# Optimization experiments

Hardware: AMD Instinct MI355X
Metric: run time of the kernel (lower is better)

The kernel has to match this reference:

```python
import jax, jax.numpy as jnp
import numpy as np
import math

B, N, D, H = 32, 577, 768, 12
HD = D // H  # 64
WS = 24  # window size
NUM_REL_DIST = (2 * WS - 1) * (2 * WS - 1) + 3  # 2212


def _build_rel_pos_index():
    ch, cw = np.arange(WS), np.arange(WS)
    coords = np.stack(np.meshgrid(ch, cw, indexing='ij'))  # [2, WS, WS]
    cf = coords.reshape(2, -1)  # [2, WS*WS]
    rel = cf[:, :, None] - cf[:, None, :]  # [2, WS*WS, WS*WS]
    rel = rel.transpose(1, 2, 0).astype(np.int64)
    rel[:, :, 0] += WS - 1
    rel[:, :, 1] += WS - 1
    rel[:, :, 0] *= 2 * WS - 1
    idx = np.zeros((WS * WS + 1, WS * WS + 1), dtype=np.int64)
    idx[1:, 1:] = rel.sum(-1)
    idx[0, 0:] = NUM_REL_DIST - 3
    idx[0:, 0] = NUM_REL_DIST - 2
    idx[0, 0] = NUM_REL_DIST - 1
    return idx.astype(np.int32)


def setup_inputs() -> dict:
    key = jax.random.key(0)
    ks = jax.random.split(key, 7)
    s = 1.0 / math.sqrt(D)
    return {
        'hidden_states': jax.random.normal(ks[0], (B, N, D), jnp.float32),
        'q_w': jax.random.normal(ks[1], (D, D), jnp.float32) * s,
        'q_b': jax.random.normal(ks[2], (D,), jnp.float32) * 0.02,
        'k_w': jax.random.normal(ks[3], (D, D), jnp.float32) * s,
        'v_w': jax.random.normal(ks[4], (D, D), jnp.float32) * s,
        'v_b': jax.random.normal(ks[5], (D,), jnp.float32) * 0.02,
        'rel_pos_table': jax.random.normal(ks[6], (NUM_REL_DIST, H), jnp.float32) * 0.02,
        'rel_pos_index': jnp.asarray(_build_rel_pos_index()),
    }


def reference(hidden_states, q_w, q_b, k_w, v_w, v_b, rel_pos_table, rel_pos_index):
    # QKV projections (torch Linear: x @ W.T + b); key has no bias
    q = hidden_states @ q_w.T + q_b  # [B,N,D]
    k = hidden_states @ k_w.T        # [B,N,D]
    v = hidden_states @ v_w.T + v_b  # [B,N,D]

    def heads(x):
        return x.reshape(B, N, H, HD).transpose(0, 2, 1, 3)  # [B,H,N,HD]

    q, k, v = heads(q), heads(k), heads(v)
    scores = jnp.einsum('bhqd,bhkd->bhqk', q, k) / math.sqrt(HD)
    # relative position bias: table lookup -> [N,N,H] -> [H,N,N]
    bias = rel_pos_table[rel_pos_index.reshape(-1)].reshape(N, N, H)
    scores = scores + bias.transpose(2, 0, 1)[None]
    probs = jax.nn.softmax(scores, axis=-1)  # dropout p=0 (eval)
    ctx = jnp.einsum('bhqk,bhkd->bhqd', probs, v)
    return ctx.transpose(0, 2, 1, 3).reshape(B, N, D)
```

## Files before the change

kernel.cpp:

```cpp
#include <hip/hip_runtime.h>
#include <hip/hip_bf16.h>

#define B_  32
#define N_  577
#define D_  768
#define H_  12
#define HD_ 64
#define M_  (B_ * N_)
#define NW_ (3 * D_)
#define VN_ 640
#define BPAD_ 640
#define SCALE_ 0.18033688f

typedef __bf16 bf16_t;
typedef __bf16 bf16x8 __attribute__((ext_vector_type(8)));
typedef __bf16 bf16x4 __attribute__((ext_vector_type(4)));
typedef float  f32x4  __attribute__((ext_vector_type(4)));

static __device__ __forceinline__ bf16x8 ldg8(const bf16_t* p) {
    return *reinterpret_cast<const bf16x8*>(p);
}

#define GPERM(r) (((r) & 32) | (((r) & 8) << 1) | (((r) & 4) << 1) | \
                  (((r) & 16) >> 2) | ((r) & 3))

#define GLOAD_LDS16(g, l)                                                     \
    __builtin_amdgcn_global_load_lds(                                         \
        (const __attribute__((address_space(1))) void*)(g),                   \
        (__attribute__((address_space(3))) void*)(l), 16, 0, 0)

__global__ void cvt_f32_bf16(const float* __restrict__ src,
                             bf16_t* __restrict__ dst, int n4) {
    int i = blockIdx.x * blockDim.x + threadIdx.x;
    if (i < n4) {
        float4 f = reinterpret_cast<const float4*>(src)[i];
        bf16x4 o;
        o.x = (bf16_t)f.x; o.y = (bf16_t)f.y; o.z = (bf16_t)f.z; o.w = (bf16_t)f.w;
        *reinterpret_cast<bf16x4*>(dst + (size_t)i * 4) = o;
    }
}

__global__ void cvt3_f32_bf16(const float* __restrict__ s0,
                              const float* __restrict__ s1,
                              const float* __restrict__ s2,
                              bf16_t* __restrict__ dst, int n4) {
    int i = blockIdx.x * blockDim.x + threadIdx.x;
    if (i < n4) {
        const float* src = blockIdx.y == 0 ? s0 : (blockIdx.y == 1 ? s1 : s2);
        float4 f = reinterpret_cast<const float4*>(src)[i];
        bf16x4 o;
        o.x = (bf16_t)f.x; o.y = (bf16_t)f.y; o.z = (bf16_t)f.z; o.w = (bf16_t)f.w;
        *reinterpret_cast<bf16x4*>(dst + (size_t)blockIdx.y * n4 * 4 + (size_t)i * 4) = o;
    }
}

__global__ void build_bias2(const float* __restrict__ table,
                            const int* __restrict__ idx,
                            float* __restrict__ bias2) {
    int q = blockIdx.x;
    int rr = q < N_ ? q : (N_ - 1);
    for (int kl = threadIdx.x; kl < BPAD_; kl += blockDim.x) {
        int s = kl & 63;
        int gk = (kl & ~63) | GPERM(s);
        if (gk < N_) {
            int id = idx[rr * N_ + gk];
            const float* trow = table + (size_t)id * H_;
#pragma unroll
            for (int h = 0; h < H_; ++h)
                bias2[((size_t)h * BPAD_ + q) * BPAD_ + kl] =
                    trow[h] * 1.44269504f;
        } else {
#pragma unroll
            for (int h = 0; h < H_; ++h)
                bias2[((size_t)h * BPAD_ + q) * BPAD_ + kl] = -1e30f;
        }
    }
}

__global__ __launch_bounds__(256) void qkv_gemm(
    const bf16_t* __restrict__ hb, const bf16_t* __restrict__ W,
    const float* __restrict__ qb, const float* __restrict__ vb,
    bf16_t* __restrict__ Q, bf16_t* __restrict__ K, bf16_t* __restrict__ VT)
{
    __shared__ __align__(16) char lds[65536];

    int tid = threadIdx.x;
    int w  = tid >> 6, l = tid & 63;
    int lr = l & 15, lg = l >> 4;
    int wm = w & 1,  wn = w >> 1;

    int wg = blockIdx.x;
    int xcd = wg & 7, pos = wg >> 3;
    const int Q8 = 2610 / 8, R8 = 2610 % 8;
    int base = xcd < R8 ? xcd * (Q8 + 1) : R8 * (Q8 + 1) + (xcd - R8) * Q8;
    int wgid = base + pos;
    int bx = wgid / 18, y = wgid - bx * 18;
    int brow = bx * 128;
    int mat = y / 6, ysub = y - mat * 6;
    int cbase = ysub * 128;

    int srow = tid >> 3;
    int sslot = (tid & 7) ^ (srow & 7);
    const bf16_t* pa[4];
    const bf16_t* pb[4];
#pragma unroll
    for (int r = 0; r < 4; ++r) {
        int ra = brow + r * 32 + srow; ra = ra < M_ ? ra : (M_ - 1);
        pa[r] = hb + (size_t)ra * D_ + sslot * 8;
        pb[r] = W + (size_t)(y * 128 + r * 32 + srow) * D_ + sslot * 8;
    }

    auto stage = [&](int buf, int k) {
#pragma unroll
        for (int r = 0; r < 4; ++r) {
            GLOAD_LDS16(pa[r] + k, lds + buf * 16384 + r * 4096 + tid * 16);
            GLOAD_LDS16(pb[r] + k, lds + 32768 + buf * 16384 + r * 4096 + tid * 16);
        }
    };

    f32x4 acc[4][4] = {};
    stage(0, 0);
    int cur = 0;
    for (int t = 0; t < 12; ++t) {
        if (t < 11) {
            stage(cur ^ 1, (t + 1) * 64);
            asm volatile("s_waitcnt vmcnt(8)" ::: "memory");
        } else {
            asm volatile("s_waitcnt vmcnt(0)" ::: "memory");
        }
        __builtin_amdgcn_s_barrier();
        __builtin_amdgcn_sched_barrier(0);

        const char* pA = lds + cur * 16384;
        const char* pB = lds + 32768 + cur * 16384;
#pragma unroll
        for (int kk = 0; kk < 2; ++kk) {
            bf16x8 af[4];
#pragma unroll
            for (int m = 0; m < 4; ++m) {
                int row = wm * 64 + m * 16 + lr;
                af[m] = *reinterpret_cast<const bf16x8*>(
                    pA + row * 128 + (((kk * 4 + lg) ^ (lr & 7)) << 4));
            }
#pragma unroll
            for (int n = 0; n < 4; ++n) {
                int row = wn * 64 + n * 16 + lr;
                bf16x8 bfr = *reinterpret_cast<const bf16x8*>(
                    pB + row * 128 + (((kk * 4 + lg) ^ (lr & 7)) << 4));
#pragma unroll
                for (int m = 0; m < 4; ++m)
                    acc[m][n] = __builtin_amdgcn_mfma_f32_16x16x32_bf16(
                        af[m], bfr, acc[m][n], 0, 0, 0);
            }
        }
        __builtin_amdgcn_sched_barrier(0);
        __builtin_amdgcn_s_barrier();
        cur ^= 1;
    }

    bf16_t* ep = (bf16_t*)lds;
    if (mat < 2) {
#pragma unroll
        for (int m = 0; m < 4; ++m)
#pragma unroll
            for (int n = 0; n < 4; ++n) {
                int col = wn * 64 + n * 16 + lr;
#pragma unroll
                for (int j = 0; j < 4; ++j) {
                    int row = wm * 64 + m * 16 + lg * 4 + j;
                    float v = acc[m][n][j];
                    v = (mat == 0) ? (v + qb[cbase + col]) * SCALE_ : v;
                    ep[row * 132 + col] = (bf16_t)v;
                }
            }
        __syncthreads();
        bf16_t* dst0 = (mat == 0) ? Q : K;
#pragma unroll
        for (int k = 0; k < 8; ++k) {
            int c = k * 256 + tid;
            int row = c >> 4, cc = c & 15;
            int grow = brow + row;
            if (grow < M_) {
                int bb = grow / N_, nn = grow - bb * N_;
                int col0 = cc * 8;
                int hh = ysub * 2 + (col0 >> 6);
                int hd0 = col0 & 63;
                bf16x8 vc = *reinterpret_cast<const bf16x8*>(ep + row * 132 + col0);
                *reinterpret_cast<bf16x8*>(
                    dst0 + ((size_t)(bb * H_ + hh) * N_ + nn) * HD_ + hd0) = vc;
            }
        }
    } else {
#pragma unroll
        for (int m = 0; m < 4; ++m)
#pragma unroll
            for (int n = 0; n < 4; ++n) {
                int col = wn * 64 + n * 16 + lr;
                float badd = vb[cbase + col];
#pragma unroll
                for (int j = 0; j < 4; ++j) {
                    int row = wm * 64 + m * 16 + lg * 4 + j;
                    ep[col * 132 + row] = (bf16_t)(acc[m][n][j] + badd);
                }
            }
        __syncthreads();
#pragma unroll
        for (int k = 0; k < 8; ++k) {
            int c = k * 256 + tid;
            int col = c >> 4, rc = c & 15;
            int grow0 = brow + rc * 8;
            int hh = ysub * 2 + (col >> 6), hd = col & 63;
            int bb = grow0 / N_, nn0 = grow0 - bb * N_;
            if (nn0 + 8 <= N_ && grow0 + 8 <= M_) {
                *reinterpret_cast<bf16x8*>(
                    VT + ((size_t)(bb * H_ + hh) * HD_ + hd) * VN_ + nn0) =
                    *reinterpret_cast<const bf16x8*>(ep + col * 132 + rc * 8);
            } else {
                for (int jj = 0; jj < 8; ++jj) {
                    int grow = grow0 + jj;
                    if (grow >= M_) break;
                    int b2 = grow / N_, n2 = grow - b2 * N_;
                    VT[((size_t)(b2 * H_ + hh) * HD_ + hd) * VN_ + n2] =
                        ep[col * 132 + rc * 8 + jj];
                }
            }
        }
    }
}

__global__ __launch_bounds__(256) void attn(
    const bf16_t* __restrict__ Q, const bf16_t* __restrict__ K,
    const bf16_t* __restrict__ VT, const float* __restrict__ bias2,
    float* __restrict__ out)
{
    __shared__ __align__(16) char Kl[2][8192];
    __shared__ __align__(16) char Vl[2][8192];

    int tid = threadIdx.x;
    int w = tid >> 6, l = tid & 63, lr = l & 15, lg = l >> 4;

    int wg = blockIdx.x;
    int wgid = (wg & 7) * 480 + (wg >> 3);
    int h = wgid / 320;
    int rem = wgid - h * 320;
    int b = rem / 10;
    int qt = rem - b * 10;

    const bf16_t* Qp = Q  + (size_t)(b * H_ + h) * N_ * HD_;
    const bf16_t* Kp = K  + (size_t)(b * H_ + h) * N_ * HD_;
    const bf16_t* Vp = VT + (size_t)(b * H_ + h) * HD_ * VN_;
    const float*  bp = bias2 + (size_t)h * BPAD_ * BPAD_;

    int q0 = qt * 64 + w * 16;
    int qrow = q0 + lr;
    int qrow_c = qrow < N_ ? qrow : (N_ - 1);
    bf16x8 aQ0 = ldg8(Qp + (size_t)qrow_c * HD_ + lg * 8);
    bf16x8 aQ1 = ldg8(Qp + (size_t)qrow_c * HD_ + 32 + lg * 8);

    bf16x8 vone;
#pragma unroll
    for (int i = 0; i < 8; ++i) vone[i] = (bf16_t)1.0f;

    int rloc = l >> 3;
    int cswz = (l & 7) ^ rloc;
    const bf16_t* Kst[2];
    const bf16_t* Vst[2];
#pragma unroll
    for (int rnd = 0; rnd < 2; ++rnd) {
        int r = rnd * 32 + w * 8 + rloc;
        int gk = GPERM(r);
        Kst[rnd] = Kp + (size_t)gk * HD_ + cswz * 8;
        Vst[rnd] = Vp + (size_t)r * VN_ + cswz * 8;
    }

    f32x4 o[4] = {};
    f32x4 osum = {};
    const int NT = 10;

    auto stageKV = [&](int buf, int k0) {
#pragma unroll
        for (int rnd = 0; rnd < 2; ++rnd)
            GLOAD_LDS16(Kst[rnd] + (size_t)k0 * HD_,
                        Kl[buf] + rnd * 4096 + w * 1024);
#pragma unroll
        for (int rnd = 0; rnd < 2; ++rnd)
            GLOAD_LDS16(Vst[rnd] + k0, Vl[buf] + rnd * 4096 + w * 1024);
    };
    auto loadBias = [&](int k0, f32x4* bbv) {
        const float* brow = bp + (size_t)(q0 + lr) * BPAD_ + k0;
#pragma unroll
        for (int kt = 0; kt < 4; ++kt)
            bbv[kt] = *reinterpret_cast<const f32x4*>(brow + kt * 16 + lg * 4);
    };

    auto tile = [&](int t, int rbuf, const f32x4* bbcur, f32x4* bbnxt) {
        int k0 = t * 64;
        if (t + 1 < NT) {
            stageKV(rbuf ^ 1, k0 + 64);
            loadBias(k0 + 64, bbnxt);
        }
        __builtin_amdgcn_sched_barrier(0);

        f32x4 s[4];
        __builtin_amdgcn_s_setprio(1);
#pragma unroll
        for (int kt = 0; kt < 4; ++kt) {
            int r = kt * 16 + lr;
            bf16x8 kf0 = *reinterpret_cast<const bf16x8*>(
                Kl[rbuf] + r * 128 + ((lg ^ (r & 7)) << 4));
            bf16x8 kf1 = *reinterpret_cast<const bf16x8*>(
                Kl[rbuf] + r * 128 + (((4 + lg) ^ (r & 7)) << 4));
            f32x4 a = __builtin_amdgcn_mfma_f32_16x16x32_bf16(
                kf0, aQ0, bbcur[kt], 0, 0, 0);
            s[kt] = __builtin_amdgcn_mfma_f32_16x16x32_bf16(kf1, aQ1, a, 0, 0, 0);
        }
        __builtin_amdgcn_s_setprio(0);

        float p[4][4];
#pragma unroll
        for (int kt = 0; kt < 4; ++kt)
#pragma unroll
            for (int j = 0; j < 4; ++j)
                p[kt][j] = __builtin_amdgcn_exp2f(s[kt][j]);

        __builtin_amdgcn_s_setprio(1);
#pragma unroll
        for (int kc = 0; kc < 2; ++kc) {
            bf16x8 aP;
            aP[0] = (bf16_t)p[2 * kc][0];
            aP[1] = (bf16_t)p[2 * kc][1];
            aP[2] = (bf16_t)p[2 * kc][2];
            aP[3] = (bf16_t)p[2 * kc][3];
            aP[4] = (bf16_t)p[2 * kc + 1][0];
            aP[5] = (bf16_t)p[2 * kc + 1][1];
            aP[6] = (bf16_t)p[2 * kc + 1][2];
            aP[7] = (bf16_t)p[2 * kc + 1][3];
            osum = __builtin_amdgcn_mfma_f32_16x16x32_bf16(aP, vone, osum, 0, 0, 0);
#pragma unroll
            for (int ft = 0; ft < 4; ++ft) {
                int d = ft * 16 + lr;
                bf16x8 bV = *reinterpret_cast<const bf16x8*>(
                    Vl[rbuf] + d * 128 + (((kc * 4 + lg) ^ (d & 7)) << 4));
                o[ft] = __builtin_amdgcn_mfma_f32_16x16x32_bf16(aP, bV, o[ft], 0, 0, 0);
            }
        }
        __builtin_amdgcn_s_setprio(0);
        __builtin_amdgcn_sched_barrier(0);

        if (t + 1 < NT) asm volatile("s_waitcnt vmcnt(4)" ::: "memory");
        else            asm volatile("s_waitcnt vmcnt(0)" ::: "memory");
        __builtin_amdgcn_s_barrier();
        __builtin_amdgcn_sched_barrier(0);
    };

    f32x4 bbA[4], bbB[4];
    stageKV(0, 0);
    loadBias(0, bbA);
    asm volatile("s_waitcnt vmcnt(4)" ::: "memory");
    __builtin_amdgcn_s_barrier();
    __builtin_amdgcn_sched_barrier(0);

    for (int tp = 0; tp < NT / 2; ++tp) {
        tile(tp * 2,     0, bbA, bbB);
        tile(tp * 2 + 1, 1, bbB, bbA);
    }

#pragma unroll
    for (int j = 0; j < 4; ++j) {
        int row = q0 + lg * 4 + j;
        if (row < N_) {
            float inv = 1.f / osum[j];
#pragma unroll
            for (int ft = 0; ft < 4; ++ft)
                out[((size_t)(b * N_ + row)) * D_ + h * HD_ + ft * 16 + lr] =
                    o[ft][j] * inv;
        }
    }
}

extern "C" void kernel_launch(void* const* d_in, const int* in_sizes, int n_in,
                              void* d_out, int out_size, void* d_ws, size_t ws_size,
                              hipStream_t stream)
{
    const float* hs    = (const float*)d_in[0];
    const float* q_w   = (const float*)d_in[1];
    const float* q_b   = (const float*)d_in[2];
    const float* k_w   = (const float*)d_in[3];
    const float* v_w   = (const float*)d_in[4];
    const float* v_b   = (const float*)d_in[5];
    const float* table = (const float*)d_in[6];
    const int*   rpi   = (const int*)d_in[7];
    float* out = (float*)d_out;

    char* ws = (char*)d_ws;
    size_t off = 0;
    auto alloc = [&](size_t bytes) {
        char* p = ws + off;
        off = (off + bytes + 255) & ~(size_t)255;
        return p;
    };
    bf16_t* hb  = (bf16_t*)alloc((size_t)M_ * D_ * 2);
    bf16_t* Wc  = (bf16_t*)alloc((size_t)NW_ * D_ * 2);
    bf16_t* Qb  = (bf16_t*)alloc((size_t)B_ * H_ * N_ * HD_ * 2);
    bf16_t* Kb  = (bf16_t*)alloc((size_t)B_ * H_ * N_ * HD_ * 2 + 16384);
    bf16_t* VTb = (bf16_t*)alloc((size_t)B_ * H_ * HD_ * VN_ * 2);
    float*  bia = (float*)alloc((size_t)H_ * BPAD_ * BPAD_ * 4);

    int n4h = M_ * D_ / 4;
    cvt_f32_bf16<<<(n4h + 255) / 256, 256, 0, stream>>>(hs, hb, n4h);
    int n4w = D_ * D_ / 4;
    cvt3_f32_bf16<<<dim3((n4w + 255) / 256, 3), 256, 0, stream>>>(
        q_w, k_w, v_w, Wc, n4w);
    build_bias2<<<BPAD_, 256, 0, stream>>>(table, rpi, bia);

    qkv_gemm<<<2610, 256, 0, stream>>>(hb, Wc, q_b, v_b, Qb, Kb, VTb);

    attn<<<3840, 256, 0, stream>>>(Qb, Kb, VTb, bia, out);
}
```

Measured before the change: 214.1 us.

## Enlarge QKV GEMM tiles to 256x256 with 512 threads and 4-stage pipeline

New measurement: 211.2 us (median of 2 runs). Within noise of the previous version (-1.4%).

```diff
diff --git a/kernel.cpp b/kernel.cpp
--- a/kernel.cpp
+++ b/kernel.cpp
@@ -77,153 +77,166 @@
     }
 }
 
-__global__ __launch_bounds__(256) void qkv_gemm(
+__global__ __launch_bounds__(512, 2) void qkv_gemm(
     const bf16_t* __restrict__ hb, const bf16_t* __restrict__ W,
     const float* __restrict__ qb, const float* __restrict__ vb,
     bf16_t* __restrict__ Q, bf16_t* __restrict__ K, bf16_t* __restrict__ VT)
 {
-    __shared__ __align__(16) char lds[65536];
+    __shared__ __align__(16) char lds[131072];
 
     int tid = threadIdx.x;
     int w  = tid >> 6, l = tid & 63;
     int lr = l & 15, lg = l >> 4;
-    int wm = w & 1,  wn = w >> 1;
+    int wm = w >> 2, wn = w & 3;
 
     int wg = blockIdx.x;
     int xcd = wg & 7, pos = wg >> 3;
-    const int Q8 = 2610 / 8, R8 = 2610 % 8;
-    int base = xcd < R8 ? xcd * (Q8 + 1) : R8 * (Q8 + 1) + (xcd - R8) * Q8;
+    int base = (xcd == 0) ? 0 : 83 + (xcd - 1) * 82;
     int wgid = base + pos;
-    int bx = wgid / 18, y = wgid - bx * 18;
-    int brow = bx * 128;
-    int mat = y / 6, ysub = y - mat * 6;
-    int cbase = ysub * 128;
-
-    int srow = tid >> 3;
-    int sslot = (tid & 7) ^ (srow & 7);
-    const bf16_t* pa[4];
-    const bf16_t* pb[4];
-#pragma unroll
-    for (int r = 0; r < 4; ++r) {
-        int ra = brow + r * 32 + srow; ra = ra < M_ ? ra : (M_ - 1);
+    int bx = wgid / 9, ct = wgid - bx * 9;
+    int brow = bx * 256;
+    int mat = ct / 3, csub = ct - mat * 3;
+    int cbase = csub * 256;
+
+    int srow = tid >> 2;
+    int sslot = (tid & 3) ^ ((srow >> 1) & 3);
+    const bf16_t* pa[2];
+    const bf16_t* pb[2];
+#pragma unroll
+    for (int r = 0; r < 2; ++r) {
+        int ra = brow + r * 128 + srow; ra = ra < M_ ? ra : (M_ - 1);
         pa[r] = hb + (size_t)ra * D_ + sslot * 8;
-        pb[r] = W + (size_t)(y * 128 + r * 32 + srow) * D_ + sslot * 8;
+        pb[r] = W + (size_t)(ct * 256 + r * 128 + srow) * D_ + sslot * 8;
     }
 
     auto stage = [&](int buf, int k) {
 #pragma unroll
-        for (int r = 0; r < 4; ++r) {
-            GLOAD_LDS16(pa[r] + k, lds + buf * 16384 + r * 4096 + tid * 16);
-            GLOAD_LDS16(pb[r] + k, lds + 32768 + buf * 16384 + r * 4096 + tid * 16);
+        for (int r = 0; r < 2; ++r) {
+            GLOAD_LDS16(pa[r] + k, lds + buf * 16384 + r * 8192 + tid * 16);
+            GLOAD_LDS16(pb[r] + k, lds + 65536 + buf * 16384 + r * 8192 + tid * 16);
         }
     };
 
-    f32x4 acc[4][4] = {};
+    f32x4 acc[8][4] = {};
     stage(0, 0);
-    int cur = 0;
-    for (int t = 0; t < 12; ++t) {
-        if (t < 11) {
-            stage(cur ^ 1, (t + 1) * 64);
-            asm volatile("s_waitcnt vmcnt(8)" ::: "memory");
-        } else {
-            asm volatile("s_waitcnt vmcnt(0)" ::: "memory");
-        }
+    stage(1, 32);
+    stage(2, 64);
+    int xsw = (lr >> 1) & 3;
+
+#pragma unroll 4
+    for (int t = 0; t < 24; ++t) {
+        if (t < 22)       asm volatile("s_waitcnt vmcnt(8)" ::: "memory");
+        else if (t == 22) asm volatile("s_waitcnt vmcnt(4)" ::: "memory");
+        else              asm volatile("s_waitcnt vmcnt(0)" ::: "memory");
         __builtin_amdgcn_s_barrier();
         __builtin_amdgcn_sched_barrier(0);
-
-        const char* pA = lds + cur * 16384;
-        const char* pB = lds + 32768 + cur * 16384;
-#pragma unroll
-        for (int kk = 0; kk < 2; ++kk) {
-            bf16x8 af[4];
-#pragma unroll
-            for (int m = 0; m < 4; ++m) {
-                int row = wm * 64 + m * 16 + lr;
-                af[m] = *reinterpret_cast<const bf16x8*>(
-                    pA + row * 128 + (((kk * 4 + lg) ^ (lr & 7)) << 4));
-            }
-#pragma unroll
-            for (int n = 0; n < 4; ++n) {
-                int row = wn * 64 + n * 16 + lr;
-                bf16x8 bfr = *reinterpret_cast<const bf16x8*>(
-                    pB + row * 128 + (((kk * 4 + lg) ^ (lr & 7)) << 4));
-#pragma unroll
-                for (int m = 0; m < 4; ++m)
-                    acc[m][n] = __builtin_amdgcn_mfma_f32_16x16x32_bf16(
-                        af[m], bfr, acc[m][n], 0, 0, 0);
-            }
-        }
-        __builtin_amdgcn_sched_barrier(0);
-        __builtin_amdgcn_s_barrier();
-        cur ^= 1;
-    }
+        if (t + 3 < 24) stage((t + 3) & 3, (t + 3) * 32);
+        __builtin_amdgcn_sched_barrier(0);
+
+        const char* pA = lds + (t & 3) * 16384;
+        const char* pB = lds + 65536 + (t & 3) * 16384;
+        bf16x8 bf[4];
+#pragma unroll
+        for (int n = 0; n < 4; ++n) {
+            int row = wn * 64 + n * 16 + lr;
+            bf[n] = *reinterpret_cast<const bf16x8*>(
+                pB + row * 64 + ((lg ^ xsw) << 4));
+        }
+        __builtin_amdgcn_s_setprio(1);
+#pragma unroll
+        for (int m = 0; m < 8; ++m) {
+            int row = wm * 128 + m * 16 + lr;
+            bf16x8 af = *reinterpret_cast<const bf16x8*>(
+                pA + row * 64 + ((lg ^ xsw) << 4));
+#pragma unroll
+            for (int n = 0; n < 4; ++n)
+                acc[m][n] = __builtin_amdgcn_mfma_f32_16x16x32_bf16(
+                    af, bf[n], acc[m][n], 0, 0, 0);
+        }
+        __builtin_amdgcn_s_setprio(0);
+        __builtin_amdgcn_sched_barrier(0);
+    }
+    __syncthreads();
 
     bf16_t* ep = (bf16_t*)lds;
     if (mat < 2) {
-#pragma unroll
-        for (int m = 0; m < 4; ++m)
-#pragma unroll
-            for (int n = 0; n < 4; ++n) {
-                int col = wn * 64 + n * 16 + lr;
-#pragma unroll
-                for (int j = 0; j < 4; ++j) {
-                    int row = wm * 64 + m * 16 + lg * 4 + j;
-                    float v = acc[m][n][j];
-                    v = (mat == 0) ? (v + qb[cbase + col]) * SCALE_ : v;
-                    ep[row * 132 + col] = (bf16_t)v;
+        bf16_t* dst0 = (mat == 0) ? Q : K;
+#pragma unroll
+        for (int hp = 0; hp < 2; ++hp) {
+            if (wm == hp) {
+#pragma unroll
+                for (int m = 0; m < 8; ++m)
+#pragma unroll
+                    for (int n = 0; n < 4; ++n) {
+                        int col = wn * 64 + n * 16 + lr;
+                        float badd = (mat == 0) ? qb[cbase + col] : 0.f;
+#pragma unroll
+                        for (int j = 0; j < 4; ++j) {
+                            int rl = m * 16 + lg * 4 + j;
+                            float v = acc[m][n][j];
+                            v = (mat == 0) ? (v + badd) * SCALE_ : v;
+                            ep[rl * 260 + col] = (bf16_t)v;
+                        }
+                    }
+            }
+            __syncthreads();
+#pragma unroll
+            for (int k = 0; k < 8; ++k) {
+                int c = k * 512 + tid;
+                int row = c >> 5, chunk = c & 31;
+                int col0 = chunk * 8;
+                int grow = brow + hp * 128 + row;
+                if (grow < M_) {
+                    int bb = grow / N_, nn = grow - bb * N_;
+                    int hh = csub * 4 + (col0 >> 6);
+                    int hd0 = col0 & 63;
+                    *reinterpret_cast<bf16x8*>(
+                        dst0 + ((size_t)(bb * H_ + hh) * N_ + nn) * HD_ + hd0) =
+                        *reinterpret_cast<const bf16x8*>(ep + row * 260 + col0);
                 }
             }
-        __syncthreads();
-        bf16_t* dst0 = (mat == 0) ? Q : K;
-#pragma unroll
-        for (int k = 0; k < 8; ++k) {
-            int c = k * 256 + tid;
-            int row = c >> 4, cc = c & 15;
-            int grow = brow + row;
-            if (grow < M_) {
-                int bb = grow / N_, nn = grow - bb * N_;
-                int col0 = cc * 8;
-                int hh = ysub * 2 + (col0 >> 6);
-                int hd0 = col0 & 63;
-                bf16x8 vc = *reinterpret_cast<const bf16x8*>(ep + row * 132 + col0);
-                *reinterpret_cast<bf16x8*>(
-                    dst0 + ((size_t)(bb * H_ + hh) * N_ + nn) * HD_ + hd0) = vc;
+            __syncthreads();
+        }
+    } else {
+#pragma unroll
+        for (int hp = 0; hp < 2; ++hp) {
+            if (wm == hp) {
+#pragma unroll
+                for (int m = 0; m < 8; ++m)
+#pragma unroll
+                    for (int n = 0; n < 4; ++n) {
+                        int col = wn * 64 + n * 16 + lr;
+                        float badd = vb[cbase + col];
+#pragma unroll
+                        for (int j = 0; j < 4; ++j) {
+                            int rl = m * 16 + lg * 4 + j;
+                            ep[col * 132 + rl] = (bf16_t)(acc[m][n][j] + badd);
+                        }
+                    }
             }
-        }
-    } else {
-#pragma unroll
-        for (int m = 0; m < 4; ++m)
-#pragma unroll
-            for (int n = 0; n < 4; ++n) {
-                int col = wn * 64 + n * 16 + lr;
-                float badd = vb[cbase + col];
-#pragma unroll
-                for (int j = 0; j < 4; ++j) {
-                    int row = wm * 64 + m * 16 + lg * 4 + j;
-                    ep[col * 132 + row] = (bf16_t)(acc[m][n][j] + badd);
+            __syncthreads();
+#pragma unroll
+            for (int k = 0; k < 8; ++k) {
+                int c = k * 512 + tid;
+                int col = c >> 4, rc = c & 15;
+                int grow0 = brow + hp * 128 + rc * 8;
+                int hh = csub * 4 + (col >> 6), hd = col & 63;
+                int bb = grow0 / N_, nn0 = grow0 - bb * N_;
+                if (nn0 + 8 <= N_ && grow0 + 8 <= M_) {
+                    *reinterpret_cast<bf16x8*>(
+                        VT + ((size_t)(bb * H_ + hh) * HD_ + hd) * VN_ + nn0) =
+                        *reinterpret_cast<const bf16x8*>(ep + col * 132 + rc * 8);
+                } else {
+                    for (int jj = 0; jj < 8; ++jj) {
+                        int grow = grow0 + jj;
+                        if (grow >= M_) break;
+                        int b2 = grow / N_, n2 = grow - b2 * N_;
+                        VT[((size_t)(b2 * H_ + hh) * HD_ + hd) * VN_ + n2] =
+                            ep[col * 132 + rc * 8 + jj];
+                    }
                 }
             }
-        __syncthreads();
-#pragma unroll
-        for (int k = 0; k < 8; ++k) {
-            int c = k * 256 + tid;
-            int col = c >> 4, rc = c & 15;
-            int grow0 = brow + rc * 8;
-            int hh = ysub * 2 + (col >> 6), hd = col & 63;
-            int bb = grow0 / N_, nn0 = grow0 - bb * N_;
-            if (nn0 + 8 <= N_ && grow0 + 8 <= M_) {
-                *reinterpret_cast<bf16x8*>(
-                    VT + ((size_t)(bb * H_ + hh) * HD_ + hd) * VN_ + nn0) =
-                    *reinterpret_cast<const bf16x8*>(ep + col * 132 + rc * 8);
-            } else {
-                for (int jj = 0; jj < 8; ++jj) {
-                    int grow = grow0 + jj;
-                    if (grow >= M_) break;
-                    int b2 = grow / N_, n2 = grow - b2 * N_;
-                    VT[((size_t)(b2 * H_ + hh) * HD_ + hd) * VN_ + n2] =
-                        ep[col * 132 + rc * 8 + jj];
-                }
-            }
+            __syncthreads();
         }
     }
 }
@@ -413,7 +426,7 @@
         q_w, k_w, v_w, Wc, n4w);
     build_bias2<<<BPAD_, 256, 0, stream>>>(table, rpi, bia);
 
-    qkv_gemm<<<2610, 256, 0, stream>>>(hb, Wc, q_b, v_b, Qb, Kb, VTb);
+    qkv_gemm<<<657, 512, 0, stream>>>(hb, Wc, q_b, v_b, Qb, Kb, VTb);
 
     attn<<<3840, 256, 0, stream>>>(Qb, Kb, VTb, bia, out);
 }
```
